# Performance work log

Measured on AMD Instinct MI355X. Metric: run time of the kernel, lower is better.

## Reference

```python
import jax, jax.numpy as jnp
import numpy as np

N_USER = 1_000_000
N_ITEM = 500_000
U_FEAT = 21
I_FEAT = 39
EMB = 64
HID = 256
BATCH = 16384


def _linear_params(key, out_f, in_f):
    kw, kb = jax.random.split(key)
    bound = 1.0 / np.sqrt(in_f)
    W = jax.random.uniform(kw, (out_f, in_f), jnp.float32, -bound, bound)
    b = jax.random.uniform(kb, (out_f,), jnp.float32, -bound, bound)
    return W, b


def setup_inputs() -> dict:
    key = jax.random.key(0)
    ks = jax.random.split(key, 10)
    user_id = jax.random.randint(ks[0], (BATCH,), 0, N_USER + 1, dtype=jnp.int64 if jax.config.jax_enable_x64 else jnp.int32)
    item_id = jax.random.randint(ks[1], (BATCH,), 0, N_ITEM + 1, dtype=jnp.int64 if jax.config.jax_enable_x64 else jnp.int32)
    user_features = jax.random.normal(ks[2], (BATCH, U_FEAT), jnp.float32)
    item_features = jax.random.normal(ks[3], (BATCH, I_FEAT), jnp.float32)
    user_emb = jax.random.normal(ks[4], (N_USER + 1, EMB), jnp.float32)
    item_emb = jax.random.normal(ks[5], (N_ITEM + 1, EMB), jnp.float32)
    W_uf, b_uf = _linear_params(ks[6], EMB, EMB + U_FEAT)
    W_if, b_if = _linear_params(ks[7], EMB, EMB + I_FEAT)
    W1, b1 = _linear_params(ks[8], HID, 2 * EMB)
    W2, b2 = _linear_params(ks[9], 1, HID)
    return {
        "user_id": user_id, "item_id": item_id,
        "user_features": user_features, "item_features": item_features,
        "user_emb": user_emb, "item_emb": item_emb,
        "W_uf": W_uf, "b_uf": b_uf, "W_if": W_if, "b_if": b_if,
        "W1": W1, "b1": b1, "W2": W2, "b2": b2,
    }


def reference(user_id, item_id, user_features, item_features,
              user_emb, item_emb, W_uf, b_uf, W_if, b_if, W1, b1, W2, b2):
    ue = user_emb[user_id]                               # [B, EMB]
    ie = item_emb[item_id]                               # [B, EMB]
    uh = jax.nn.relu(jnp.concatenate([ue, user_features], axis=1))
    uh = uh @ W_uf.T + b_uf + ue                         # linear + residual
    ih = jax.nn.relu(jnp.concatenate([ie, item_features], axis=1))
    ih = ih @ W_if.T + b_if + ie
    h = jax.nn.relu(jnp.concatenate([uh, ih], axis=1))   # [B, 2*EMB]
    h = jax.nn.relu(h @ W1.T + b1)                       # dropout(p=0) is identity
    return h @ W2.T + b2                                 # [B, 1]
```

## Files before the change

### kernel.cpp

```cpp
#include <hip/hip_runtime.h>

#define TB      64
#define THREADS 512
#define EMB     64
#define UFEAT   21
#define IFEAT   39
#define KXU     85
#define KXI     103
#define HW      128
#define HID     256
#define XU_S    89
#define XI_S    105
#define H_S     129

template<int K, int S>
__device__ __forceinline__ void layer_in(const float (*__restrict__ X)[S], int lane, int o0,
                                         const float* __restrict__ W,
                                         const float* __restrict__ b,
                                         float (*__restrict__ H)[H_S], int hoff)
{
    float acc[16];
    const float* x = X[lane];
    #pragma unroll
    for (int j = 0; j < 16; ++j) acc[j] = b[o0 + j] + x[o0 + j];
    #pragma unroll 4
    for (int k = 0; k < K; ++k) {
        const float a = fmaxf(x[k], 0.f);
        #pragma unroll
        for (int j = 0; j < 16; ++j)
            acc[j] = fmaf(a, W[(o0 + j) * K + k], acc[j]);
    }
    #pragma unroll
    for (int j = 0; j < 16; ++j)
        H[lane][hoff + o0 + j] = fmaxf(acc[j], 0.f);
}

__global__ __launch_bounds__(THREADS, 1)
void rec_fused(const int*   __restrict__ user_id,  const int*   __restrict__ item_id,
               const float* __restrict__ user_feat, const float* __restrict__ item_feat,
               const float* __restrict__ user_emb,  const float* __restrict__ item_emb,
               const float* __restrict__ W_uf, const float* __restrict__ b_uf,
               const float* __restrict__ W_if, const float* __restrict__ b_if,
               const float* __restrict__ W1,  const float* __restrict__ b1,
               const float* __restrict__ W2,  const float* __restrict__ b2,
               float* __restrict__ out)
{
    __shared__ float sXU[TB][XU_S];
    __shared__ float sXI[TB][XI_S];
    __shared__ float sH [TB][H_S];
    __shared__ float sOut[8][TB];

    const int t  = threadIdx.x;
    const int s0 = blockIdx.x * TB;

    #pragma unroll 2
    for (int i = t; i < TB * (EMB / 4); i += THREADS) {
        const int r = i >> 4, c = (i & 15) * 4;
        const int uid = user_id[s0 + r];
        const float4 v = *reinterpret_cast<const float4*>(user_emb + uid * EMB + c);
        sXU[r][c] = v.x; sXU[r][c + 1] = v.y; sXU[r][c + 2] = v.z; sXU[r][c + 3] = v.w;
    }
    #pragma unroll 2
    for (int i = t; i < TB * (EMB / 4); i += THREADS) {
        const int r = i >> 4, c = (i & 15) * 4;
        const int iid = item_id[s0 + r];
        const float4 v = *reinterpret_cast<const float4*>(item_emb + iid * EMB + c);
        sXI[r][c] = v.x; sXI[r][c + 1] = v.y; sXI[r][c + 2] = v.z; sXI[r][c + 3] = v.w;
    }
    for (int i = t; i < TB * UFEAT; i += THREADS)
        sXU[i / UFEAT][EMB + i % UFEAT] = user_feat[s0 * UFEAT + i];
    for (int i = t; i < TB * IFEAT; i += THREADS)
        sXI[i / IFEAT][EMB + i % IFEAT] = item_feat[s0 * IFEAT + i];
    __syncthreads();

    const int wave = __builtin_amdgcn_readfirstlane(t >> 6);
    const int lane = t & 63;

    if (wave < 4) layer_in<KXU, XU_S>(sXU, lane, wave * 16,       W_uf, b_uf, sH, 0);
    else          layer_in<KXI, XI_S>(sXI, lane, (wave - 4) * 16, W_if, b_if, sH, EMB);
    __syncthreads();

    {
        const int o0 = wave * 32;
        float acc[32];
        #pragma unroll
        for (int j = 0; j < 32; ++j) acc[j] = b1[o0 + j];
        const float* h = sH[lane];
        #pragma unroll 2
        for (int k = 0; k < HW; ++k) {
            const float a = h[k];
            #pragma unroll
            for (int j = 0; j < 32; ++j)
                acc[j] = fmaf(a, W1[(o0 + j) * HW + k], acc[j]);
        }
        float op = 0.f;
        #pragma unroll
        for (int j = 0; j < 32; ++j)
            op += fmaxf(acc[j], 0.f) * W2[o0 + j];
        sOut[wave][lane] = op;
    }
    __syncthreads();

    if (t < TB) {
        float r = b2[0];
        #pragma unroll
        for (int w = 0; w < 8; ++w) r += sOut[w][t];
        out[s0 + t] = r;
    }
}

extern "C" void kernel_launch(void* const* d_in, const int* in_sizes, int n_in,
                              void* d_out, int out_size, void* d_ws, size_t ws_size,
                              hipStream_t stream) {
    const int*   user_id   = (const int*)  d_in[0];
    const int*   item_id   = (const int*)  d_in[1];
    const float* user_feat = (const float*)d_in[2];
    const float* item_feat = (const float*)d_in[3];
    const float* user_emb  = (const float*)d_in[4];
    const float* item_emb  = (const float*)d_in[5];
    const float* W_uf      = (const float*)d_in[6];
    const float* b_uf      = (const float*)d_in[7];
    const float* W_if      = (const float*)d_in[8];
    const float* b_if      = (const float*)d_in[9];
    const float* W1        = (const float*)d_in[10];
    const float* b1        = (const float*)d_in[11];
    const float* W2        = (const float*)d_in[12];
    const float* b2        = (const float*)d_in[13];
    float* out = (float*)d_out;

    const int blocks = 16384 / TB;
    rec_fused<<<blocks, THREADS, 0, stream>>>(
        user_id, item_id, user_feat, item_feat, user_emb, item_emb,
        W_uf, b_uf, W_if, b_if, W1, b1, W2, b2, out);
}
```

Before: 445.6 us.

## Double threads per block, alias hidden buffer onto input smem, raise occupancy

Doubles the block to 1024 threads (16 waves), so each wave computes 8 outputs in the input layers and 16 outputs of the hidden layer instead of 16 and 32. This cuts per-thread accumulator registers and allows more resident waves via launch_bounds(…,4). The hidden activation buffer now reuses the input shared-memory region, which needs an extra barrier, and the embedding gather becomes a single unlooped pass. The intent is better latency hiding through higher occupancy. In exchange, W loads are spread across more waves and the kernel pays one more sync.

```diff
diff --git a/kernel.cpp b/kernel.cpp
--- a/kernel.cpp
+++ b/kernel.cpp
@@ -1,41 +1,36 @@
 #include <hip/hip_runtime.h>
 
 #define TB      64
-#define THREADS 512
+#define THREADS 1024
+#define NWAVE   16
 #define EMB     64
 #define UFEAT   21
 #define IFEAT   39
 #define KXU     85
 #define KXI     103
 #define HW      128
-#define HID     256
 #define XU_S    89
 #define XI_S    105
 #define H_S     129
 
-template<int K, int S>
-__device__ __forceinline__ void layer_in(const float (*__restrict__ X)[S], int lane, int o0,
-                                         const float* __restrict__ W,
-                                         const float* __restrict__ b,
-                                         float (*__restrict__ H)[H_S], int hoff)
+template<int K>
+__device__ __forceinline__ void layer8(const float* __restrict__ x, int o0,
+                                       const float* __restrict__ W,
+                                       const float* __restrict__ b,
+                                       float acc[8])
 {
-    float acc[16];
-    const float* x = X[lane];
     #pragma unroll
-    for (int j = 0; j < 16; ++j) acc[j] = b[o0 + j] + x[o0 + j];
+    for (int j = 0; j < 8; ++j) acc[j] = b[o0 + j] + x[o0 + j];
     #pragma unroll 4
     for (int k = 0; k < K; ++k) {
         const float a = fmaxf(x[k], 0.f);
         #pragma unroll
-        for (int j = 0; j < 16; ++j)
+        for (int j = 0; j < 8; ++j)
             acc[j] = fmaf(a, W[(o0 + j) * K + k], acc[j]);
     }
-    #pragma unroll
-    for (int j = 0; j < 16; ++j)
-        H[lane][hoff + o0 + j] = fmaxf(acc[j], 0.f);
 }
 
-__global__ __launch_bounds__(THREADS, 1)
+__global__ __launch_bounds__(THREADS, 4)
 void rec_fused(const int*   __restrict__ user_id,  const int*   __restrict__ item_id,
                const float* __restrict__ user_feat, const float* __restrict__ item_feat,
                const float* __restrict__ user_emb,  const float* __restrict__ item_emb,
@@ -45,58 +40,64 @@
                const float* __restrict__ W2,  const float* __restrict__ b2,
                float* __restrict__ out)
 {
-    __shared__ float sXU[TB][XU_S];
-    __shared__ float sXI[TB][XI_S];
-    __shared__ float sH [TB][H_S];
-    __shared__ float sOut[8][TB];
+    __shared__ float smem[TB * XU_S + TB * XI_S];
+    __shared__ float sOut[NWAVE][TB];
 
     const int t  = threadIdx.x;
     const int s0 = blockIdx.x * TB;
+    float* sXU = smem;
+    float* sXI = smem + TB * XU_S;
 
-    #pragma unroll 2
-    for (int i = t; i < TB * (EMB / 4); i += THREADS) {
-        const int r = i >> 4, c = (i & 15) * 4;
+    {
+        const int r = t >> 4, c = (t & 15) << 2;
         const int uid = user_id[s0 + r];
-        const float4 v = *reinterpret_cast<const float4*>(user_emb + uid * EMB + c);
-        sXU[r][c] = v.x; sXU[r][c + 1] = v.y; sXU[r][c + 2] = v.z; sXU[r][c + 3] = v.w;
-    }
-    #pragma unroll 2
-    for (int i = t; i < TB * (EMB / 4); i += THREADS) {
-        const int r = i >> 4, c = (i & 15) * 4;
         const int iid = item_id[s0 + r];
+        const float4 u = *reinterpret_cast<const float4*>(user_emb + uid * EMB + c);
         const float4 v = *reinterpret_cast<const float4*>(item_emb + iid * EMB + c);
-        sXI[r][c] = v.x; sXI[r][c + 1] = v.y; sXI[r][c + 2] = v.z; sXI[r][c + 3] = v.w;
+        float* pu = sXU + r * XU_S + c;
+        pu[0] = u.x; pu[1] = u.y; pu[2] = u.z; pu[3] = u.w;
+        float* pi = sXI + r * XI_S + c;
+        pi[0] = v.x; pi[1] = v.y; pi[2] = v.z; pi[3] = v.w;
     }
     for (int i = t; i < TB * UFEAT; i += THREADS)
-        sXU[i / UFEAT][EMB + i % UFEAT] = user_feat[s0 * UFEAT + i];
+        sXU[(i / UFEAT) * XU_S + EMB + i % UFEAT] = user_feat[s0 * UFEAT + i];
     for (int i = t; i < TB * IFEAT; i += THREADS)
-        sXI[i / IFEAT][EMB + i % IFEAT] = item_feat[s0 * IFEAT + i];
+        sXI[(i / IFEAT) * XI_S + EMB + i % IFEAT] = item_feat[s0 * IFEAT + i];
     __syncthreads();
 
     const int wave = __builtin_amdgcn_readfirstlane(t >> 6);
     const int lane = t & 63;
 
-    if (wave < 4) layer_in<KXU, XU_S>(sXU, lane, wave * 16,       W_uf, b_uf, sH, 0);
-    else          layer_in<KXI, XI_S>(sXI, lane, (wave - 4) * 16, W_if, b_if, sH, EMB);
+    float acc[8];
+    if (wave < 8) layer8<KXU>(sXU + lane * XU_S, wave * 8,       W_uf, b_uf, acc);
+    else          layer8<KXI>(sXI + lane * XI_S, (wave - 8) * 8, W_if, b_if, acc);
     __syncthreads();
 
     {
-        const int o0 = wave * 32;
-        float acc[32];
+        float* Hrow = smem + lane * H_S;
+        const int hoff = (wave < 8) ? wave * 8 : EMB + (wave - 8) * 8;
         #pragma unroll
-        for (int j = 0; j < 32; ++j) acc[j] = b1[o0 + j];
-        const float* h = sH[lane];
-        #pragma unroll 2
+        for (int j = 0; j < 8; ++j) Hrow[hoff + j] = fmaxf(acc[j], 0.f);
+    }
+    __syncthreads();
+
+    {
+        const int o0 = wave * 16;
+        float a3[16];
+        #pragma unroll
+        for (int j = 0; j < 16; ++j) a3[j] = b1[o0 + j];
+        const float* h = smem + lane * H_S;
+        #pragma unroll 4
         for (int k = 0; k < HW; ++k) {
             const float a = h[k];
             #pragma unroll
-            for (int j = 0; j < 32; ++j)
-                acc[j] = fmaf(a, W1[(o0 + j) * HW + k], acc[j]);
+            for (int j = 0; j < 16; ++j)
+                a3[j] = fmaf(a, W1[(o0 + j) * HW + k], a3[j]);
         }
         float op = 0.f;
         #pragma unroll
-        for (int j = 0; j < 32; ++j)
-            op += fmaxf(acc[j], 0.f) * W2[o0 + j];
+        for (int j = 0; j < 16; ++j)
+            op = fmaf(fmaxf(a3[j], 0.f), W2[o0 + j], op);
         sOut[wave][lane] = op;
     }
     __syncthreads();
@@ -104,7 +105,7 @@
     if (t < TB) {
         float r = b2[0];
         #pragma unroll
-        for (int w = 0; w < 8; ++w) r += sOut[w][t];
+        for (int w = 0; w < NWAVE; ++w) r += sOut[w][t];
         out[s0 + t] = r;
     }
 }
```

Result: faster. 408.4 us (median of 2 runs) (-8.4%).
